# Kernel optimization log

Hardware: AMD Instinct MI355X
Metric: run time of the kernel (lower is better)

## Reference

```python
import jax, jax.numpy as jnp
import numpy as np

SIGMA = 1.0
E_THETA = 0.1
E_ALPHA = 1.0
E_G = 1.0
WIN = 11  # window size hard-coded in the torch loop
B = 4096
T = 750


def _pad(x):
    # Faithful to torch: x[:,0].repeat(1,6).reshape(B,6) == tile-then-reshape
    # (element (b,c) = x[(6b+c) % B, 0], a broadcast bug preserved on purpose).
    b = x.shape[0]
    front = jnp.tile(x[:, 0], 6).reshape(b, 6)
    back = jnp.tile(x[:, -1], 6).reshape(b, 6)
    # middle assignment 6:-5 overwrites index T+5, so only back[:,1:] survives
    return jnp.concatenate([front, x, back[:, 1:]], axis=1)  # (B, T+11)


def setup_inputs() -> dict:
    key = jax.random.key(0)
    k1, k2 = jax.random.split(key)
    actioness = jax.random.uniform(k1, (B, T), dtype=jnp.float32)
    actioness_2 = jax.random.uniform(k2, (B, T), dtype=jnp.float32)
    return {"actioness": actioness, "actioness_2": actioness_2}


def reference(actioness, actioness_2):
    b, t = actioness.shape
    a3 = _pad(actioness_2)   # (B, T+11)
    a4 = _pad(actioness)     # (B, T+11)

    idx = jnp.arange(t)[:, None] + jnp.arange(WIN)[None, :]  # (T, 11)
    a4_win = a4[:, idx]  # (B, T, 11)
    a3_win = a3[:, idx]  # (B, T, 11)

    # torch repeat(1,11).reshape(B,11): element (b,c) = actioness[(11b+c)%B, i]
    R = (WIN * jnp.arange(b)[:, None] + jnp.arange(WIN)[None, :]) % b  # (B, 11)
    tiled = jnp.transpose(actioness[R], (0, 2, 1))  # (B, T, 11)
    max_w = jnp.max(tiled - a4_win, axis=2)  # (B, T); independent of j

    # ||a0[:,i] - detach(a4)[:,i+j]||_2^2 over batch dim -> scalar per (i, j)
    ns = jnp.sum((actioness[:, :, None] - jax.lax.stop_gradient(a4_win)) ** 2, axis=0)  # (T, 11)

    g_mw2 = E_G * max_w * max_w  # (B, T)
    expo = jax.nn.relu(ns[None, :, :] - g_mw2[:, :, None]) + g_mw2[:, :, None]  # (B, T, 11)
    w = jnp.exp(-expo / (2.0 * SIGMA * SIGMA))  # (B, T, 11)

    d2 = jnp.abs(actioness_2[:, :, None] - a3_win)  # (B, T, 11)
    # sum over i,j of mean over batch == total sum / B
    loss = jnp.sum(w * d2) / b

    diff = actioness - actioness_2
    loss = loss + E_THETA * jnp.mean(jnp.sum(diff * diff, axis=1))
    return loss * E_ALPHA
```

## Files before the change

kernel.cpp:

```cpp
#include <hip/hip_runtime.h>

#define BB 4096
#define TT 750
#define NS_STRIDE 768
#define NBLK 768
#define NRED 33

#define NSP_OFF   0
#define EDGE_OFF  (4608 * 64)
#define ENS_OFF   (EDGE_OFF + 128)
#define SLOT_OFF  (ENS_OFF + 8448)
#define FLAG_OFF  (SLOT_OFF + 768)
#define RSLOT_OFF (FLAG_OFF + 64)

__global__ __launch_bounds__(256, 4) void k_A(const float* __restrict__ a,
                                              const float* __restrict__ a2,
                                              float* __restrict__ ws) {
    float* ns_p   = ws + NSP_OFF;
    float* edge_c = ws + EDGE_OFF;
    float* rslots = ws + RSLOT_OFF;
    __shared__ float smem[2432];
    __shared__ float swred[4];
    __shared__ float swred2[4];
    const int b = blockIdx.x, tid = threadIdx.x;
    const int x = b % 12, y = b / 12;
    const int t0 = x * 64, i0 = y * 64;
    const int tl = tid & 63, ig = tid >> 6;

    float acc[6] = {0.f, 0.f, 0.f, 0.f, 0.f, 0.f};
    float racc = 0.f;

    for (int h = 0; h < 2; ++h) {
        for (int l = tid; l < 32 * 74; l += 256) {
            int r = l / 74, c = l - r * 74;
            int gc = t0 - 6 + c;
            float v = 0.f;
            if (gc >= 0 && gc < TT) v = a[(i0 + h * 32 + r) * TT + gc];
            smem[r * 76 + c] = v;
        }
        __syncthreads();
        if (x == 0) {
            for (int r = ig; r < 32; r += 4) {
                float xx = smem[r * 76 + tl + 6];
#pragma unroll
                for (int k = 0; k < 6; ++k) {
                    float d = xx - smem[r * 76 + tl + k];
                    if (tl + k >= 6) acc[k] += d * d;
                }
            }
        } else if (x == 11) {
            const int t = t0 + tl;
            if (t < TT) {
                for (int r = ig; r < 32; r += 4) {
                    float xx = smem[r * 76 + tl + 6];
#pragma unroll
                    for (int k = 0; k < 6; ++k) {
                        float d = xx - smem[r * 76 + tl + k];
                        acc[k] += d * d;
                    }
                }
            }
        } else {
            for (int r = ig; r < 32; r += 4) {
                float xx = smem[r * 76 + tl + 6];
#pragma unroll
                for (int k = 0; k < 6; ++k) {
                    float d = xx - smem[r * 76 + tl + k];
                    acc[k] += d * d;
                }
            }
        }
        {
            const int t = t0 + tl;
            if (t < TT) {
                for (int r = ig; r < 32; r += 4) {
                    float d = smem[r * 76 + tl + 6] - a2[(i0 + h * 32 + r) * TT + t];
                    racc += d * d;
                }
            }
        }
        __syncthreads();
    }

#pragma unroll
    for (int k = 0; k < 6; ++k) smem[ig * 384 + tl * 6 + k] = acc[k];
    __syncthreads();

    for (int l = tid; l < 384; l += 256) {
        float s = smem[l] + smem[384 + l] + smem[768 + l] + smem[1152 + l];
        ns_p[(size_t)(x * 384 + l) * 64 + y] = s;
    }

    for (int off = 32; off > 0; off >>= 1) racc += __shfl_down(racc, off, 64);
    if (tl == 0) swred2[ig] = racc;
    __syncthreads();
    if (tid == 0)
        rslots[b] = 0.1f * (swred2[0] + swred2[1] + swred2[2] + swred2[3]);

    if (b < 124) {
        const int q = b >> 2, ch = b & 3;
        int t = 0, k = 0;
        if (q < 21) {
            int idx = q;
            for (int tt = 0; tt < 6; ++tt) {
                int c = 6 - tt;
                if (idx < c) { t = tt; k = idx; break; }
                idx -= c;
            }
        } else {
            int idx = q - 21;
            for (int tt = 746; tt < 750; ++tt) {
                int c = tt - 745;
                if (idx < c) { t = tt; k = (11 - c) + idx; break; }
                idx -= c;
            }
        }
        const int p = t + k;
        float s = 0.f;
        int i = ch * 1024 + tid;
#pragma unroll
        for (int it = 0; it < 4; ++it, i += 256) {
            float xv = a[i * TT + t];
            float v = (p < 6) ? a[((6 * i + p) & (BB - 1)) * TT]
                              : a[((6 * i + (p - 755)) & (BB - 1)) * TT + (TT - 1)];
            float d = xv - v;
            s += d * d;
        }
        for (int off = 32; off > 0; off >>= 1) s += __shfl_down(s, off, 64);
        if (tl == 0) swred[ig] = s;
        __syncthreads();
        if (tid == 0)
            edge_c[q * 4 + ch] = swred[0] + swred[1] + swred[2] + swred[3];
    }
}

__global__ __launch_bounds__(256) void k_B(const float* __restrict__ ws_ro,
                                           float* __restrict__ ws) {
    const float* ns_p   = ws_ro + NSP_OFF;
    const float* edge_c = ws_ro + EDGE_OFF;
    float* ens   = ws + ENS_OFF;
    int*   flags = (int*)(ws + FLAG_OFF);
    __shared__ int swf[4];
    const int b = blockIdx.x, tid = threadIdx.x;
    const int l = b * 256 + tid;
    const int k = l / NS_STRIDE;
    const int t = l - k * NS_STRIDE;
    float e = 0.f;
    if (t < TT) {
        if (k == 6) {
            e = 1.0f;
        } else {
            int row;
            if (k < 6) {
                row = (t >> 6) * 384 + (t & 63) * 6 + k;
            } else {
                int q = t + k - 6;
                int kk = 12 - k;
                row = (q >> 6) * 384 + (q & 63) * 6 + kk;
            }
            const float4* pp4 = (const float4*)(ns_p + (size_t)row * 64);
            float s = 0.f;
#pragma unroll
            for (int j = 0; j < 16; ++j) {
                float4 v = pp4[j];
                s += v.x + v.y + v.z + v.w;
            }
            const int p = t + k;
            if (p < 6) {
                int idx = t * 6 - t * (t - 1) / 2 + k;
                s += edge_c[idx * 4 + 0] + edge_c[idx * 4 + 1] +
                     edge_c[idx * 4 + 2] + edge_c[idx * 4 + 3];
            } else if (p >= 756) {
                int idx = 21 + (t - 746) * (t - 745) / 2 + (k - (756 - t));
                s += edge_c[idx * 4 + 0] + edge_c[idx * 4 + 1] +
                     edge_c[idx * 4 + 2] + edge_c[idx * 4 + 3];
            }
            e = __expf(-0.5f * s);
        }
    }
    ens[l] = e;
    unsigned long long anyb = __ballot(e > 0.f && k != 6);
    if ((tid & 63) == 0) swf[tid >> 6] = (anyb != 0ull);
    __syncthreads();
    if (tid == 0) flags[b] = swf[0] | swf[1] | swf[2] | swf[3];
}

__global__ __launch_bounds__(256, 4) void k_C(const float* __restrict__ a,
                                              const float* __restrict__ a2,
                                              float* __restrict__ ws) {
    const float* ens   = ws + ENS_OFF;
    const int*   flags = (const int*)(ws + FLAG_OFF);
    float* slots = ws + SLOT_OFF;
    const int b = blockIdx.x, tid = threadIdx.x;

    int flag = 0;
    for (int j = 0; j < NRED; ++j) flag |= flags[j];

    if (flag == 0) {
        if (tid == 0) slots[b] = 0.f;
        return;
    }

    __shared__ float s_a4[268];
    __shared__ float s_a3[268];
    __shared__ float swred[4];
    const int x = b % 3;
    const int y = b / 3;
    const int t0 = x * 256;
    const int t = t0 + tid;

    float partial = 0.f;
    for (int ii = 0; ii < 16; ++ii) {
        const int i = y * 16 + ii;
        __syncthreads();
        for (int c = tid; c < 266; c += 256) {
            int p = t0 + c;
            float v4, v3;
            if (p < 6) {
                int r = (6 * i + p) & (BB - 1);
                v4 = a[r * TT];
                v3 = a2[r * TT];
            } else if (p < 756) {
                v4 = a[i * TT + p - 6];
                v3 = a2[i * TT + p - 6];
            } else {
                int r = (6 * i + (p - 755)) & (BB - 1);
                v4 = a[r * TT + (TT - 1)];
                v3 = a2[r * TT + (TT - 1)];
            }
            s_a4[c] = v4;
            s_a3[c] = v3;
        }
        __syncthreads();
        if (t < TT) {
            const float s2 = s_a3[tid + 6];
            float mw = -1e30f;
            float acc_d[11], acc_e[11];
#pragma unroll
            for (int k = 0; k < 11; ++k) {
                float a4v = s_a4[tid + k];
                float a3v = s_a3[tid + k];
                int rr = (11 * i + k) & (BB - 1);
                float tv = a[rr * TT + t];
                mw = fmaxf(mw, tv - a4v);
                acc_d[k] = fabsf(s2 - a3v);
                acc_e[k] = ens[k * NS_STRIDE + t];
            }
            float g = mw * mw;
            float eg = __expf(-0.5f * g);
            float acc = 0.f;
#pragma unroll
            for (int k = 0; k < 11; ++k) acc += fminf(acc_e[k], eg) * acc_d[k];
            partial += acc;
        }
    }

    for (int off = 32; off > 0; off >>= 1) partial += __shfl_down(partial, off, 64);
    if ((tid & 63) == 0) swred[tid >> 6] = partial;
    __syncthreads();
    if (tid == 0)
        slots[b] = swred[0] + swred[1] + swred[2] + swred[3];
}

__global__ __launch_bounds__(256) void k_D(const float* __restrict__ ws_ro,
                                           float* __restrict__ out) {
    const float* slots  = ws_ro + SLOT_OFF;
    const float* rslots = ws_ro + RSLOT_OFF;
    __shared__ float fred[4];
    const int tid = threadIdx.x;
    float v = slots[tid] + slots[tid + 256] + slots[tid + 512]
            + rslots[tid] + rslots[tid + 256] + rslots[tid + 512];
    for (int off = 32; off > 0; off >>= 1) v += __shfl_down(v, off, 64);
    if ((tid & 63) == 0) fred[tid >> 6] = v;
    __syncthreads();
    if (tid == 0)
        out[0] = (fred[0] + fred[1] + fred[2] + fred[3]) * (1.0f / BB);
}

extern "C" void kernel_launch(void* const* d_in, const int* in_sizes, int n_in,
                              void* d_out, int out_size, void* d_ws, size_t ws_size,
                              hipStream_t stream) {
    const float* a  = (const float*)d_in[0];
    const float* a2 = (const float*)d_in[1];
    float* ws  = (float*)d_ws;
    float* out = (float*)d_out;

    k_A<<<NBLK, 256, 0, stream>>>(a, a2, ws);
    k_B<<<NRED, 256, 0, stream>>>(ws, ws);
    k_C<<<NBLK, 256, 0, stream>>>(a, a2, ws);
    k_D<<<1, 256, 0, stream>>>(ws, out);
}
```

Before: 89.93 us.

## Fuse four kernels into one cooperative kernel with grid syncs

Merges the partial-reduction, exp-table, main loss and final reduction kernels into a single cooperative launch that separates phases with grid.sync. The exp-table phase is spread across all 768 blocks using 16-lane shuffle reductions instead of 33 blocks with serial loops. Per-block slots are replaced by a global atomic flag and an atomic accumulator. This removes three kernel launch gaps and tail effects, but adds grid-wide barrier cost, a non-deterministic atomic float sum, and requires all 768 blocks to be co-resident.

```diff
diff --git a/kernel.cpp b/kernel.cpp
--- a/kernel.cpp
+++ b/kernel.cpp
@@ -1,56 +1,77 @@
 #include <hip/hip_runtime.h>
+#include <hip/hip_cooperative_groups.h>
+
+namespace cg = cooperative_groups;
 
 #define BB 4096
 #define TT 750
 #define NS_STRIDE 768
 #define NBLK 768
-#define NRED 33
 
 #define NSP_OFF   0
 #define EDGE_OFF  (4608 * 64)
 #define ENS_OFF   (EDGE_OFF + 128)
-#define SLOT_OFF  (ENS_OFF + 8448)
-#define FLAG_OFF  (SLOT_OFF + 768)
-#define RSLOT_OFF (FLAG_OFF + 64)
-
-__global__ __launch_bounds__(256, 4) void k_A(const float* __restrict__ a,
-                                              const float* __restrict__ a2,
-                                              float* __restrict__ ws) {
+#define GFLAG_OFF (ENS_OFF + 8448)
+#define WACC_OFF  (GFLAG_OFF + 16)
+#define RSLOT_OFF (WACC_OFF + 16)
+
+__global__ __launch_bounds__(256, 4) void k_fused(const float* __restrict__ a,
+                                                  const float* __restrict__ a2,
+                                                  float* __restrict__ ws,
+                                                  float* __restrict__ out) {
+    cg::grid_group grid = cg::this_grid();
     float* ns_p   = ws + NSP_OFF;
     float* edge_c = ws + EDGE_OFF;
+    float* ens    = ws + ENS_OFF;
+    int*   gflag  = (int*)(ws + GFLAG_OFF);
+    float* wacc   = ws + WACC_OFF;
     float* rslots = ws + RSLOT_OFF;
     __shared__ float smem[2432];
     __shared__ float swred[4];
     __shared__ float swred2[4];
     const int b = blockIdx.x, tid = threadIdx.x;
-    const int x = b % 12, y = b / 12;
-    const int t0 = x * 64, i0 = y * 64;
-    const int tl = tid & 63, ig = tid >> 6;
-
-    float acc[6] = {0.f, 0.f, 0.f, 0.f, 0.f, 0.f};
-    float racc = 0.f;
-
-    for (int h = 0; h < 2; ++h) {
-        for (int l = tid; l < 32 * 74; l += 256) {
-            int r = l / 74, c = l - r * 74;
-            int gc = t0 - 6 + c;
-            float v = 0.f;
-            if (gc >= 0 && gc < TT) v = a[(i0 + h * 32 + r) * TT + gc];
-            smem[r * 76 + c] = v;
-        }
-        __syncthreads();
-        if (x == 0) {
-            for (int r = ig; r < 32; r += 4) {
-                float xx = smem[r * 76 + tl + 6];
-#pragma unroll
-                for (int k = 0; k < 6; ++k) {
-                    float d = xx - smem[r * 76 + tl + k];
-                    if (tl + k >= 6) acc[k] += d * d;
-                }
-            }
-        } else if (x == 11) {
-            const int t = t0 + tl;
-            if (t < TT) {
+
+    if (b == 0 && tid == 0) { *gflag = 0; *wacc = 0.f; }
+
+    {
+        const int x = b % 12, y = b / 12;
+        const int t0 = x * 64, i0 = y * 64;
+        const int tl = tid & 63, ig = tid >> 6;
+
+        float acc[6] = {0.f, 0.f, 0.f, 0.f, 0.f, 0.f};
+        float racc = 0.f;
+
+        for (int h = 0; h < 2; ++h) {
+            for (int l = tid; l < 32 * 74; l += 256) {
+                int r = l / 74, c = l - r * 74;
+                int gc = t0 - 6 + c;
+                float v = 0.f;
+                if (gc >= 0 && gc < TT) v = a[(i0 + h * 32 + r) * TT + gc];
+                smem[r * 76 + c] = v;
+            }
+            __syncthreads();
+            if (x == 0) {
+                for (int r = ig; r < 32; r += 4) {
+                    float xx = smem[r * 76 + tl + 6];
+#pragma unroll
+                    for (int k = 0; k < 6; ++k) {
+                        float d = xx - smem[r * 76 + tl + k];
+                        if (tl + k >= 6) acc[k] += d * d;
+                    }
+                }
+            } else if (x == 11) {
+                const int t = t0 + tl;
+                if (t < TT) {
+                    for (int r = ig; r < 32; r += 4) {
+                        float xx = smem[r * 76 + tl + 6];
+#pragma unroll
+                        for (int k = 0; k < 6; ++k) {
+                            float d = xx - smem[r * 76 + tl + k];
+                            acc[k] += d * d;
+                        }
+                    }
+                }
+            } else {
                 for (int r = ig; r < 32; r += 4) {
                     float xx = smem[r * 76 + tl + 6];
 #pragma unroll
@@ -60,221 +81,194 @@
                     }
                 }
             }
-        } else {
-            for (int r = ig; r < 32; r += 4) {
-                float xx = smem[r * 76 + tl + 6];
-#pragma unroll
-                for (int k = 0; k < 6; ++k) {
-                    float d = xx - smem[r * 76 + tl + k];
-                    acc[k] += d * d;
-                }
-            }
-        }
-        {
-            const int t = t0 + tl;
+            {
+                const int t = t0 + tl;
+                if (t < TT) {
+                    for (int r = ig; r < 32; r += 4) {
+                        float d = smem[r * 76 + tl + 6] - a2[(i0 + h * 32 + r) * TT + t];
+                        racc += d * d;
+                    }
+                }
+            }
+            __syncthreads();
+        }
+
+#pragma unroll
+        for (int k = 0; k < 6; ++k) smem[ig * 384 + tl * 6 + k] = acc[k];
+        __syncthreads();
+
+        for (int l = tid; l < 384; l += 256) {
+            float s = smem[l] + smem[384 + l] + smem[768 + l] + smem[1152 + l];
+            ns_p[(size_t)(x * 384 + l) * 64 + y] = s;
+        }
+
+        for (int off = 32; off > 0; off >>= 1) racc += __shfl_down(racc, off, 64);
+        if (tl == 0) swred2[ig] = racc;
+        __syncthreads();
+        if (tid == 0)
+            rslots[b] = 0.1f * (swred2[0] + swred2[1] + swred2[2] + swred2[3]);
+
+        if (b < 124) {
+            const int q = b >> 2, ch = b & 3;
+            int t = 0, k = 0;
+            if (q < 21) {
+                int idx = q;
+                for (int tt = 0; tt < 6; ++tt) {
+                    int c = 6 - tt;
+                    if (idx < c) { t = tt; k = idx; break; }
+                    idx -= c;
+                }
+            } else {
+                int idx = q - 21;
+                for (int tt = 746; tt < 750; ++tt) {
+                    int c = tt - 745;
+                    if (idx < c) { t = tt; k = (11 - c) + idx; break; }
+                    idx -= c;
+                }
+            }
+            const int p = t + k;
+            float s = 0.f;
+            int i = ch * 1024 + tid;
+#pragma unroll
+            for (int it = 0; it < 4; ++it, i += 256) {
+                float xv = a[i * TT + t];
+                float v = (p < 6) ? a[((6 * i + p) & (BB - 1)) * TT]
+                                  : a[((6 * i + (p - 755)) & (BB - 1)) * TT + (TT - 1)];
+                float d = xv - v;
+                s += d * d;
+            }
+            for (int off = 32; off > 0; off >>= 1) s += __shfl_down(s, off, 64);
+            if (tl == 0) swred[ig] = s;
+            __syncthreads();
+            if (tid == 0)
+                edge_c[q * 4 + ch] = swred[0] + swred[1] + swred[2] + swred[3];
+        }
+    }
+
+    grid.sync();
+
+    if (tid < 176) {
+        const int j = tid >> 4, l16 = tid & 15;
+        const int l = b * 11 + j;
+        const int k = l / NS_STRIDE;
+        const int t = l - k * NS_STRIDE;
+        float e = 0.f;
+        if (t < TT) {
+            if (k == 6) {
+                e = 1.0f;
+            } else {
+                int row;
+                if (k < 6) {
+                    row = (t >> 6) * 384 + (t & 63) * 6 + k;
+                } else {
+                    int q = t + k - 6;
+                    int kk = 12 - k;
+                    row = (q >> 6) * 384 + (q & 63) * 6 + kk;
+                }
+                const float4 v = ((const float4*)(ns_p + (size_t)row * 64))[l16];
+                float s = v.x + v.y + v.z + v.w;
+                s += __shfl_down(s, 8, 16);
+                s += __shfl_down(s, 4, 16);
+                s += __shfl_down(s, 2, 16);
+                s += __shfl_down(s, 1, 16);
+                if (l16 == 0) {
+                    const int p = t + k;
+                    if (p < 6) {
+                        int idx = t * 6 - t * (t - 1) / 2 + k;
+                        s += edge_c[idx * 4 + 0] + edge_c[idx * 4 + 1] +
+                             edge_c[idx * 4 + 2] + edge_c[idx * 4 + 3];
+                    } else if (p >= 756) {
+                        int idx = 21 + (t - 746) * (t - 745) / 2 + (k - (756 - t));
+                        s += edge_c[idx * 4 + 0] + edge_c[idx * 4 + 1] +
+                             edge_c[idx * 4 + 2] + edge_c[idx * 4 + 3];
+                    }
+                    e = __expf(-0.5f * s);
+                }
+            }
+        }
+        if (l16 == 0) {
+            ens[l] = e;
+            if (e > 0.f && k != 6) atomicOr(gflag, 1);
+        }
+    }
+
+    grid.sync();
+
+    const int flag = __hip_atomic_load(gflag, __ATOMIC_ACQUIRE, __HIP_MEMORY_SCOPE_AGENT);
+
+    if (flag != 0) {
+        float* s_a4 = smem;
+        float* s_a3 = smem + 272;
+        const int x = b % 3;
+        const int y = b / 3;
+        const int t0 = x * 256;
+        const int t = t0 + tid;
+        float partial = 0.f;
+        for (int ii = 0; ii < 16; ++ii) {
+            const int i = y * 16 + ii;
+            __syncthreads();
+            for (int c = tid; c < 266; c += 256) {
+                int p = t0 + c;
+                float v4, v3;
+                if (p < 6) {
+                    int r = (6 * i + p) & (BB - 1);
+                    v4 = a[r * TT];
+                    v3 = a2[r * TT];
+                } else if (p < 756) {
+                    v4 = a[i * TT + p - 6];
+                    v3 = a2[i * TT + p - 6];
+                } else {
+                    int r = (6 * i + (p - 755)) & (BB - 1);
+                    v4 = a[r * TT + (TT - 1)];
+                    v3 = a2[r * TT + (TT - 1)];
+                }
+                s_a4[c] = v4;
+                s_a3[c] = v3;
+            }
+            __syncthreads();
             if (t < TT) {
-                for (int r = ig; r < 32; r += 4) {
-                    float d = smem[r * 76 + tl + 6] - a2[(i0 + h * 32 + r) * TT + t];
-                    racc += d * d;
-                }
-            }
-        }
-        __syncthreads();
-    }
-
-#pragma unroll
-    for (int k = 0; k < 6; ++k) smem[ig * 384 + tl * 6 + k] = acc[k];
-    __syncthreads();
-
-    for (int l = tid; l < 384; l += 256) {
-        float s = smem[l] + smem[384 + l] + smem[768 + l] + smem[1152 + l];
-        ns_p[(size_t)(x * 384 + l) * 64 + y] = s;
-    }
-
-    for (int off = 32; off > 0; off >>= 1) racc += __shfl_down(racc, off, 64);
-    if (tl == 0) swred2[ig] = racc;
-    __syncthreads();
-    if (tid == 0)
-        rslots[b] = 0.1f * (swred2[0] + swred2[1] + swred2[2] + swred2[3]);
-
-    if (b < 124) {
-        const int q = b >> 2, ch = b & 3;
-        int t = 0, k = 0;
-        if (q < 21) {
-            int idx = q;
-            for (int tt = 0; tt < 6; ++tt) {
-                int c = 6 - tt;
-                if (idx < c) { t = tt; k = idx; break; }
-                idx -= c;
-            }
-        } else {
-            int idx = q - 21;
-            for (int tt = 746; tt < 750; ++tt) {
-                int c = tt - 745;
-                if (idx < c) { t = tt; k = (11 - c) + idx; break; }
-                idx -= c;
-            }
-        }
-        const int p = t + k;
-        float s = 0.f;
-        int i = ch * 1024 + tid;
-#pragma unroll
-        for (int it = 0; it < 4; ++it, i += 256) {
-            float xv = a[i * TT + t];
-            float v = (p < 6) ? a[((6 * i + p) & (BB - 1)) * TT]
-                              : a[((6 * i + (p - 755)) & (BB - 1)) * TT + (TT - 1)];
-            float d = xv - v;
-            s += d * d;
-        }
-        for (int off = 32; off > 0; off >>= 1) s += __shfl_down(s, off, 64);
-        if (tl == 0) swred[ig] = s;
-        __syncthreads();
-        if (tid == 0)
-            edge_c[q * 4 + ch] = swred[0] + swred[1] + swred[2] + swred[3];
-    }
-}
-
-__global__ __launch_bounds__(256) void k_B(const float* __restrict__ ws_ro,
-                                           float* __restrict__ ws) {
-    const float* ns_p   = ws_ro + NSP_OFF;
-    const float* edge_c = ws_ro + EDGE_OFF;
-    float* ens   = ws + ENS_OFF;
-    int*   flags = (int*)(ws + FLAG_OFF);
-    __shared__ int swf[4];
-    const int b = blockIdx.x, tid = threadIdx.x;
-    const int l = b * 256 + tid;
-    const int k = l / NS_STRIDE;
-    const int t = l - k * NS_STRIDE;
-    float e = 0.f;
-    if (t < TT) {
-        if (k == 6) {
-            e = 1.0f;
-        } else {
-            int row;
-            if (k < 6) {
-                row = (t >> 6) * 384 + (t & 63) * 6 + k;
-            } else {
-                int q = t + k - 6;
-                int kk = 12 - k;
-                row = (q >> 6) * 384 + (q & 63) * 6 + kk;
-            }
-            const float4* pp4 = (const float4*)(ns_p + (size_t)row * 64);
-            float s = 0.f;
-#pragma unroll
-            for (int j = 0; j < 16; ++j) {
-                float4 v = pp4[j];
-                s += v.x + v.y + v.z + v.w;
-            }
-            const int p = t + k;
-            if (p < 6) {
-                int idx = t * 6 - t * (t - 1) / 2 + k;
-                s += edge_c[idx * 4 + 0] + edge_c[idx * 4 + 1] +
-                     edge_c[idx * 4 + 2] + edge_c[idx * 4 + 3];
-            } else if (p >= 756) {
-                int idx = 21 + (t - 746) * (t - 745) / 2 + (k - (756 - t));
-                s += edge_c[idx * 4 + 0] + edge_c[idx * 4 + 1] +
-                     edge_c[idx * 4 + 2] + edge_c[idx * 4 + 3];
-            }
-            e = __expf(-0.5f * s);
-        }
-    }
-    ens[l] = e;
-    unsigned long long anyb = __ballot(e > 0.f && k != 6);
-    if ((tid & 63) == 0) swf[tid >> 6] = (anyb != 0ull);
-    __syncthreads();
-    if (tid == 0) flags[b] = swf[0] | swf[1] | swf[2] | swf[3];
-}
-
-__global__ __launch_bounds__(256, 4) void k_C(const float* __restrict__ a,
-                                              const float* __restrict__ a2,
-                                              float* __restrict__ ws) {
-    const float* ens   = ws + ENS_OFF;
-    const int*   flags = (const int*)(ws + FLAG_OFF);
-    float* slots = ws + SLOT_OFF;
-    const int b = blockIdx.x, tid = threadIdx.x;
-
-    int flag = 0;
-    for (int j = 0; j < NRED; ++j) flag |= flags[j];
-
-    if (flag == 0) {
-        if (tid == 0) slots[b] = 0.f;
-        return;
-    }
-
-    __shared__ float s_a4[268];
-    __shared__ float s_a3[268];
-    __shared__ float swred[4];
-    const int x = b % 3;
-    const int y = b / 3;
-    const int t0 = x * 256;
-    const int t = t0 + tid;
-
-    float partial = 0.f;
-    for (int ii = 0; ii < 16; ++ii) {
-        const int i = y * 16 + ii;
-        __syncthreads();
-        for (int c = tid; c < 266; c += 256) {
-            int p = t0 + c;
-            float v4, v3;
-            if (p < 6) {
-                int r = (6 * i + p) & (BB - 1);
-                v4 = a[r * TT];
-                v3 = a2[r * TT];
-            } else if (p < 756) {
-                v4 = a[i * TT + p - 6];
-                v3 = a2[i * TT + p - 6];
-            } else {
-                int r = (6 * i + (p - 755)) & (BB - 1);
-                v4 = a[r * TT + (TT - 1)];
-                v3 = a2[r * TT + (TT - 1)];
-            }
-            s_a4[c] = v4;
-            s_a3[c] = v3;
-        }
-        __syncthreads();
-        if (t < TT) {
-            const float s2 = s_a3[tid + 6];
-            float mw = -1e30f;
-            float acc_d[11], acc_e[11];
-#pragma unroll
-            for (int k = 0; k < 11; ++k) {
-                float a4v = s_a4[tid + k];
-                float a3v = s_a3[tid + k];
-                int rr = (11 * i + k) & (BB - 1);
-                float tv = a[rr * TT + t];
-                mw = fmaxf(mw, tv - a4v);
-                acc_d[k] = fabsf(s2 - a3v);
-                acc_e[k] = ens[k * NS_STRIDE + t];
-            }
-            float g = mw * mw;
-            float eg = __expf(-0.5f * g);
-            float acc = 0.f;
-#pragma unroll
-            for (int k = 0; k < 11; ++k) acc += fminf(acc_e[k], eg) * acc_d[k];
-            partial += acc;
-        }
-    }
-
-    for (int off = 32; off > 0; off >>= 1) partial += __shfl_down(partial, off, 64);
-    if ((tid & 63) == 0) swred[tid >> 6] = partial;
-    __syncthreads();
-    if (tid == 0)
-        slots[b] = swred[0] + swred[1] + swred[2] + swred[3];
-}
-
-__global__ __launch_bounds__(256) void k_D(const float* __restrict__ ws_ro,
-                                           float* __restrict__ out) {
-    const float* slots  = ws_ro + SLOT_OFF;
-    const float* rslots = ws_ro + RSLOT_OFF;
-    __shared__ float fred[4];
-    const int tid = threadIdx.x;
-    float v = slots[tid] + slots[tid + 256] + slots[tid + 512]
-            + rslots[tid] + rslots[tid + 256] + rslots[tid + 512];
-    for (int off = 32; off > 0; off >>= 1) v += __shfl_down(v, off, 64);
-    if ((tid & 63) == 0) fred[tid >> 6] = v;
-    __syncthreads();
-    if (tid == 0)
-        out[0] = (fred[0] + fred[1] + fred[2] + fred[3]) * (1.0f / BB);
+                const float s2 = s_a3[tid + 6];
+                float mw = -1e30f;
+                float acc_d[11], acc_e[11];
+#pragma unroll
+                for (int k = 0; k < 11; ++k) {
+                    float a4v = s_a4[tid + k];
+                    float a3v = s_a3[tid + k];
+                    int rr = (11 * i + k) & (BB - 1);
+                    float tv = a[rr * TT + t];
+                    mw = fmaxf(mw, tv - a4v);
+                    acc_d[k] = fabsf(s2 - a3v);
+                    acc_e[k] = ens[k * NS_STRIDE + t];
+                }
+                float g = mw * mw;
+                float eg = __expf(-0.5f * g);
+                float acc = 0.f;
+#pragma unroll
+                for (int k = 0; k < 11; ++k) acc += fminf(acc_e[k], eg) * acc_d[k];
+                partial += acc;
+            }
+        }
+        for (int off = 32; off > 0; off >>= 1) partial += __shfl_down(partial, off, 64);
+        __syncthreads();
+        if ((tid & 63) == 0) swred[tid >> 6] = partial;
+        __syncthreads();
+        if (tid == 0) atomicAdd(wacc, swred[0] + swred[1] + swred[2] + swred[3]);
+        grid.sync();
+    }
+
+    if (b == 0) {
+        float v = rslots[tid] + rslots[tid + 256] + rslots[tid + 512];
+        for (int off = 32; off > 0; off >>= 1) v += __shfl_down(v, off, 64);
+        __syncthreads();
+        if ((tid & 63) == 0) swred2[tid >> 6] = v;
+        __syncthreads();
+        if (tid == 0) {
+            float tot = swred2[0] + swred2[1] + swred2[2] + swred2[3];
+            if (flag != 0)
+                tot += __hip_atomic_load(wacc, __ATOMIC_ACQUIRE, __HIP_MEMORY_SCOPE_AGENT);
+            out[0] = tot * (1.0f / BB);
+        }
+    }
 }
 
 extern "C" void kernel_launch(void* const* d_in, const int* in_sizes, int n_in,
@@ -284,9 +278,6 @@
     const float* a2 = (const float*)d_in[1];
     float* ws  = (float*)d_ws;
     float* out = (float*)d_out;
-
-    k_A<<<NBLK, 256, 0, stream>>>(a, a2, ws);
-    k_B<<<NRED, 256, 0, stream>>>(ws, ws);
-    k_C<<<NBLK, 256, 0, stream>>>(a, a2, ws);
-    k_D<<<1, 256, 0, stream>>>(ws, out);
+    void* args[] = { (void*)&a, (void*)&a2, (void*)&ws, (void*)&out };
+    hipLaunchCooperativeKernel(k_fused, dim3(NBLK), dim3(256), args, 0, stream);
 }
```

Result: slower. 309.7 us (+244.4%).
